# Kernel tuning notes

Measured on AMD Instinct MI355X. Metric: run time of the kernel, lower is better.

Reference implementation:

```python
import jax, jax.numpy as jnp
import numpy as np

N = 8192
F_IN = 2048
F_OUT = 2048
ALPHA = 0.1
NEG_BIG = -9.0e15


def setup_inputs() -> dict:
    key = jax.random.key(0)
    k1, k2, k3, k4 = jax.random.split(key, 4)
    inp = jax.random.normal(k1, (N, F_IN), dtype=jnp.float32)
    adj = jax.random.uniform(k2, (N, N), dtype=jnp.float32)
    # xavier_normal_ with gain=1.414
    std_w = 1.414 * np.sqrt(2.0 / (F_IN + F_OUT))
    W = jax.random.normal(k3, (F_IN, F_OUT), dtype=jnp.float32) * std_w
    std_a = 1.414 * np.sqrt(2.0 / (2 * F_OUT + 1))
    a = jax.random.normal(k4, (2 * F_OUT, 1), dtype=jnp.float32) * std_a
    return {"input": inp, "adj": adj, "W": W, "a": a}


def reference(input, adj, W, a):
    # h: [N, F_OUT]
    h = input @ W
    n = adj.shape[0]
    # e[i,j] = leakyrelu(a1 . h_i + a2 . h_j)  (equivalent to the repeat/cat formulation)
    a1 = a[:F_OUT, 0]  # [F_OUT]
    a2 = a[F_OUT:, 0]  # [F_OUT]
    s1 = h @ a1  # [N]
    s2 = h @ a2  # [N]
    e = jax.nn.leaky_relu(s1[:, None] + s2[None, :], negative_slope=ALPHA)  # [N, N]
    # the layer masks with an identity matrix (adj_ = eye), not adj
    mask = jnp.eye(n, dtype=e.dtype)
    scores = jnp.where(mask > 0, e, jnp.full_like(e, NEG_BIG))
    attention = jax.nn.softmax(scores, axis=1)
    # dropout is identity in eval mode
    h_prime = attention @ h  # [N, F_OUT]
    return jax.nn.elu(h_prime)
```

## Files before the change

kernel.cpp:

```cpp
#include <hip/hip_runtime.h>
#include <stdint.h>
#include <math.h>

#define NROW 8192
#define KDIM 2048
#define NDIM 2048

typedef __attribute__((ext_vector_type(8))) short bf16x8;
typedef __attribute__((ext_vector_type(4))) float f32x4;

__device__ __forceinline__ unsigned short f32_to_bf16(float f) {
    union { float f; unsigned int u; } v; v.f = f;
    unsigned int u = v.u;
    unsigned int r = u + 0x7FFFu + ((u >> 16) & 1u);
    return (unsigned short)(r >> 16);
}

__global__ void cvt_bf16_kernel(const float* __restrict__ in,
                                unsigned short* __restrict__ out) {
    int i = (blockIdx.x * 256 + threadIdx.x) * 4;
    float4 f = *(const float4*)(in + i);
    ushort4 o;
    o.x = f32_to_bf16(f.x);
    o.y = f32_to_bf16(f.y);
    o.z = f32_to_bf16(f.z);
    o.w = f32_to_bf16(f.w);
    *(ushort4*)(out + i) = o;
}

__global__ void cvt_transpose_kernel(const float* __restrict__ W,
                                     unsigned short* __restrict__ Wt) {
    __shared__ float tile[32][33];
    int tx = threadIdx.x, ty = threadIdx.y;
    int x0 = blockIdx.x * 32, y0 = blockIdx.y * 32;
    #pragma unroll
    for (int j = 0; j < 32; j += 8)
        tile[ty + j][tx] = W[(size_t)(y0 + ty + j) * NDIM + x0 + tx];
    __syncthreads();
    #pragma unroll
    for (int j = 0; j < 32; j += 8)
        Wt[(size_t)(x0 + ty + j) * KDIM + y0 + tx] = f32_to_bf16(tile[tx][ty + j]);
}

#define BM 128
#define BN 128
#define BK 32

__device__ __forceinline__ void async_ld16(const unsigned short* g, unsigned short* l) {
    __builtin_amdgcn_global_load_lds(
        (const __attribute__((address_space(1))) void*)g,
        (__attribute__((address_space(3))) void*)l,
        16, 0, 0);
}

__global__ __launch_bounds__(256)
void gemm_bf16_elu(const unsigned short* __restrict__ A,
                   const unsigned short* __restrict__ Bt,
                   float* __restrict__ C) {
    __shared__ unsigned short As[BM * BK];
    __shared__ unsigned short Bs[BN * BK];

    const int tid  = threadIdx.x;
    const int wave = tid >> 6;
    const int lane = tid & 63;
    const int quad = lane >> 4;
    const int lo   = lane & 15;

    const int m0 = blockIdx.y * BM;
    const int n0 = blockIdx.x * BN;
    const int wm = (wave >> 1) * 64;
    const int wn = (wave & 1) * 64;

    const int g0 = tid, g1 = tid + 256;
    const unsigned short* gA0 = A  + (size_t)(m0 + (g0 >> 2)) * KDIM + (g0 & 3) * 8;
    const unsigned short* gA1 = A  + (size_t)(m0 + (g1 >> 2)) * KDIM + (g1 & 3) * 8;
    const unsigned short* gB0 = Bt + (size_t)(n0 + (g0 >> 2)) * KDIM + (g0 & 3) * 8;
    const unsigned short* gB1 = Bt + (size_t)(n0 + (g1 >> 2)) * KDIM + (g1 & 3) * 8;
    unsigned short* lA0 = As + g0 * 8;
    unsigned short* lA1 = As + g1 * 8;
    unsigned short* lB0 = Bs + g0 * 8;
    unsigned short* lB1 = Bs + g1 * 8;

    f32x4 acc[4][4];
    #pragma unroll
    for (int i = 0; i < 4; ++i)
        #pragma unroll
        for (int j = 0; j < 4; ++j) {
            f32x4 z = {0.f, 0.f, 0.f, 0.f};
            acc[i][j] = z;
        }

    for (int k0 = 0; k0 < KDIM; k0 += BK) {
        async_ld16(gA0 + k0, lA0);
        async_ld16(gA1 + k0, lA1);
        async_ld16(gB0 + k0, lB0);
        async_ld16(gB1 + k0, lB1);
        __syncthreads();

        bf16x8 af[4], bg[4];
        #pragma unroll
        for (int i = 0; i < 4; ++i)
            af[i] = *(const bf16x8*)(As + (wm + i * 16 + lo) * BK + quad * 8);
        #pragma unroll
        for (int j = 0; j < 4; ++j)
            bg[j] = *(const bf16x8*)(Bs + (wn + j * 16 + lo) * BK + quad * 8);

        #pragma unroll
        for (int i = 0; i < 4; ++i)
            #pragma unroll
            for (int j = 0; j < 4; ++j)
                acc[i][j] = __builtin_amdgcn_mfma_f32_16x16x32_bf16(
                    af[i], bg[j], acc[i][j], 0, 0, 0);

        __syncthreads();
    }

    #pragma unroll
    for (int i = 0; i < 4; ++i) {
        #pragma unroll
        for (int r = 0; r < 4; ++r) {
            int m = m0 + wm + i * 16 + quad * 4 + r;
            float* crow = C + (size_t)m * NDIM + n0 + wn + lo;
            #pragma unroll
            for (int j = 0; j < 4; ++j) {
                float v = acc[i][j][r];
                crow[j * 16] = (v > 0.f) ? v : (__expf(v) - 1.f);
            }
        }
    }
}

extern "C" void kernel_launch(void* const* d_in, const int* in_sizes, int n_in,
                              void* d_out, int out_size, void* d_ws, size_t ws_size,
                              hipStream_t stream) {
    const float* input = (const float*)d_in[0];
    const float* W     = (const float*)d_in[2];
    float* out = (float*)d_out;

    unsigned short* Abf = (unsigned short*)d_ws;
    unsigned short* Wt  = Abf + (size_t)NROW * KDIM;

    cvt_bf16_kernel<<<(NROW * KDIM) / 4 / 256, 256, 0, stream>>>(input, Abf);

    cvt_transpose_kernel<<<dim3(NDIM / 32, KDIM / 32), dim3(32, 8), 0, stream>>>(W, Wt);

    gemm_bf16_elu<<<dim3(NDIM / BN, NROW / BM), 256, 0, stream>>>(Abf, Wt, out);
}
```

Baseline: 454.8 us.

## Switch GEMM to 32x32x16 MFMA with BK=64 and fuse prep kernels

Replaces the 16x16x32 MFMA tiling with 32x32x16 MFMA instructions (2x2 per wave), doubles the K tile to 64 to halve barrier count per K, and merges the bf16 conversion and W transpose into one launch. Aims to raise MFMA efficiency and cut LDS read traffic and sync/launch overhead. Larger LDS tile with 128-byte row stride may increase bank conflicts.

```diff
diff --git a/kernel.cpp b/kernel.cpp
--- a/kernel.cpp
+++ b/kernel.cpp
@@ -6,8 +6,8 @@
 #define KDIM 2048
 #define NDIM 2048
 
-typedef __attribute__((ext_vector_type(8))) short bf16x8;
-typedef __attribute__((ext_vector_type(4))) float f32x4;
+typedef __attribute__((ext_vector_type(8)))  short bf16x8;
+typedef __attribute__((ext_vector_type(16))) float f32x16;
 
 __device__ __forceinline__ unsigned short f32_to_bf16(float f) {
     union { float f; unsigned int u; } v; v.f = f;
@@ -16,35 +16,42 @@
     return (unsigned short)(r >> 16);
 }
 
-__global__ void cvt_bf16_kernel(const float* __restrict__ in,
-                                unsigned short* __restrict__ out) {
-    int i = (blockIdx.x * 256 + threadIdx.x) * 4;
-    float4 f = *(const float4*)(in + i);
-    ushort4 o;
-    o.x = f32_to_bf16(f.x);
-    o.y = f32_to_bf16(f.y);
-    o.z = f32_to_bf16(f.z);
-    o.w = f32_to_bf16(f.w);
-    *(ushort4*)(out + i) = o;
-}
+#define CVT_BLOCKS (NROW * KDIM / 4 / 256)
+#define TRN_BLOCKS ((NDIM / 32) * (KDIM / 32))
 
-__global__ void cvt_transpose_kernel(const float* __restrict__ W,
-                                     unsigned short* __restrict__ Wt) {
+__global__ void prep_kernel(const float* __restrict__ in,
+                            unsigned short* __restrict__ Abf,
+                            const float* __restrict__ W,
+                            unsigned short* __restrict__ Wt) {
     __shared__ float tile[32][33];
-    int tx = threadIdx.x, ty = threadIdx.y;
-    int x0 = blockIdx.x * 32, y0 = blockIdx.y * 32;
-    #pragma unroll
-    for (int j = 0; j < 32; j += 8)
-        tile[ty + j][tx] = W[(size_t)(y0 + ty + j) * NDIM + x0 + tx];
-    __syncthreads();
-    #pragma unroll
-    for (int j = 0; j < 32; j += 8)
-        Wt[(size_t)(x0 + ty + j) * KDIM + y0 + tx] = f32_to_bf16(tile[tx][ty + j]);
+    int tid = threadIdx.x;
+    if (blockIdx.x < CVT_BLOCKS) {
+        int i = (blockIdx.x * 256 + tid) * 4;
+        float4 f = *(const float4*)(in + i);
+        ushort4 o;
+        o.x = f32_to_bf16(f.x);
+        o.y = f32_to_bf16(f.y);
+        o.z = f32_to_bf16(f.z);
+        o.w = f32_to_bf16(f.w);
+        *(ushort4*)(Abf + i) = o;
+    } else {
+        int b = blockIdx.x - CVT_BLOCKS;
+        int x0 = (b & 63) * 32;
+        int y0 = (b >> 6) * 32;
+        int tx = tid & 31, ty = tid >> 5;
+        #pragma unroll
+        for (int j = 0; j < 32; j += 8)
+            tile[ty + j][tx] = W[(size_t)(y0 + ty + j) * NDIM + x0 + tx];
+        __syncthreads();
+        #pragma unroll
+        for (int j = 0; j < 32; j += 8)
+            Wt[(size_t)(x0 + ty + j) * KDIM + y0 + tx] = f32_to_bf16(tile[tx][ty + j]);
+    }
 }
 
 #define BM 128
 #define BN 128
-#define BK 32
+#define BK 64
 
 __device__ __forceinline__ void async_ld16(const unsigned short* g, unsigned short* l) {
     __builtin_amdgcn_global_load_lds(
@@ -63,71 +70,76 @@
     const int tid  = threadIdx.x;
     const int wave = tid >> 6;
     const int lane = tid & 63;
-    const int quad = lane >> 4;
-    const int lo   = lane & 15;
+    const int half = lane >> 5;
+    const int l32  = lane & 31;
 
     const int m0 = blockIdx.y * BM;
     const int n0 = blockIdx.x * BN;
     const int wm = (wave >> 1) * 64;
     const int wn = (wave & 1) * 64;
 
-    const int g0 = tid, g1 = tid + 256;
-    const unsigned short* gA0 = A  + (size_t)(m0 + (g0 >> 2)) * KDIM + (g0 & 3) * 8;
-    const unsigned short* gA1 = A  + (size_t)(m0 + (g1 >> 2)) * KDIM + (g1 & 3) * 8;
-    const unsigned short* gB0 = Bt + (size_t)(n0 + (g0 >> 2)) * KDIM + (g0 & 3) * 8;
-    const unsigned short* gB1 = Bt + (size_t)(n0 + (g1 >> 2)) * KDIM + (g1 & 3) * 8;
-    unsigned short* lA0 = As + g0 * 8;
-    unsigned short* lA1 = As + g1 * 8;
-    unsigned short* lB0 = Bs + g0 * 8;
-    unsigned short* lB1 = Bs + g1 * 8;
+    const unsigned short* gA[4];
+    const unsigned short* gB[4];
+    unsigned short* lA[4];
+    unsigned short* lB[4];
+    #pragma unroll
+    for (int c = 0; c < 4; ++c) {
+        int g = tid + c * 256;
+        gA[c] = A  + (size_t)(m0 + (g >> 3)) * KDIM + (g & 7) * 8;
+        gB[c] = Bt + (size_t)(n0 + (g >> 3)) * KDIM + (g & 7) * 8;
+        lA[c] = As + g * 8;
+        lB[c] = Bs + g * 8;
+    }
 
-    f32x4 acc[4][4];
+    f32x16 acc[2][2];
     #pragma unroll
-    for (int i = 0; i < 4; ++i)
+    for (int i = 0; i < 2; ++i)
         #pragma unroll
-        for (int j = 0; j < 4; ++j) {
-            f32x4 z = {0.f, 0.f, 0.f, 0.f};
+        for (int j = 0; j < 2; ++j) {
+            f32x16 z = {0.f,0.f,0.f,0.f,0.f,0.f,0.f,0.f,
+                        0.f,0.f,0.f,0.f,0.f,0.f,0.f,0.f};
             acc[i][j] = z;
         }
 
     for (int k0 = 0; k0 < KDIM; k0 += BK) {
-        async_ld16(gA0 + k0, lA0);
-        async_ld16(gA1 + k0, lA1);
-        async_ld16(gB0 + k0, lB0);
-        async_ld16(gB1 + k0, lB1);
+        #pragma unroll
+        for (int c = 0; c < 4; ++c) {
+            async_ld16(gA[c] + k0, lA[c]);
+            async_ld16(gB[c] + k0, lB[c]);
+        }
         __syncthreads();
 
-        bf16x8 af[4], bg[4];
         #pragma unroll
-        for (int i = 0; i < 4; ++i)
-            af[i] = *(const bf16x8*)(As + (wm + i * 16 + lo) * BK + quad * 8);
-        #pragma unroll
-        for (int j = 0; j < 4; ++j)
-            bg[j] = *(const bf16x8*)(Bs + (wn + j * 16 + lo) * BK + quad * 8);
-
-        #pragma unroll
-        for (int i = 0; i < 4; ++i)
+        for (int kh = 0; kh < 4; ++kh) {
+            bf16x8 af[2], bg[2];
             #pragma unroll
-            for (int j = 0; j < 4; ++j)
-                acc[i][j] = __builtin_amdgcn_mfma_f32_16x16x32_bf16(
-                    af[i], bg[j], acc[i][j], 0, 0, 0);
-
+            for (int i = 0; i < 2; ++i)
+                af[i] = *(const bf16x8*)(As + (wm + i * 32 + l32) * BK + kh * 16 + half * 8);
+            #pragma unroll
+            for (int j = 0; j < 2; ++j)
+                bg[j] = *(const bf16x8*)(Bs + (wn + j * 32 + l32) * BK + kh * 16 + half * 8);
+            #pragma unroll
+            for (int i = 0; i < 2; ++i)
+                #pragma unroll
+                for (int j = 0; j < 2; ++j)
+                    acc[i][j] = __builtin_amdgcn_mfma_f32_32x32x16_bf16(
+                        af[i], bg[j], acc[i][j], 0, 0, 0);
+        }
         __syncthreads();
     }
 
     #pragma unroll
-    for (int i = 0; i < 4; ++i) {
+    for (int i = 0; i < 2; ++i)
         #pragma unroll
-        for (int r = 0; r < 4; ++r) {
-            int m = m0 + wm + i * 16 + quad * 4 + r;
-            float* crow = C + (size_t)m * NDIM + n0 + wn + lo;
+        for (int j = 0; j < 2; ++j)
             #pragma unroll
-            for (int j = 0; j < 4; ++j) {
+            for (int r = 0; r < 16; ++r) {
+                int row = (r & 3) + 8 * (r >> 2) + 4 * half;
+                int m = m0 + wm + i * 32 + row;
+                int col = n0 + wn + j * 32 + l32;
                 float v = acc[i][j][r];
-                crow[j * 16] = (v > 0.f) ? v : (__expf(v) - 1.f);
+                C[(size_t)m * NDIM + col] = (v > 0.f) ? v : (__expf(v) - 1.f);
             }
-        }
-    }
 }
 
 extern "C" void kernel_launch(void* const* d_in, const int* in_sizes, int n_in,
@@ -140,9 +152,6 @@
     unsigned short* Abf = (unsigned short*)d_ws;
     unsigned short* Wt  = Abf + (size_t)NROW * KDIM;
 
-    cvt_bf16_kernel<<<(NROW * KDIM) / 4 / 256, 256, 0, stream>>>(input, Abf);
-
-    cvt_transpose_kernel<<<dim3(NDIM / 32, KDIM / 32), dim3(32, 8), 0, stream>>>(W, Wt);
-
+    prep_kernel<<<CVT_BLOCKS + TRN_BLOCKS, 256, 0, stream>>>(input, Abf, W, Wt);
     gemm_bf16_elu<<<dim3(NDIM / BN, NROW / BM), 256, 0, stream>>>(Abf, Wt, out);
 }
```

Result: slower. 492.3 us (+8.2%).
